# Kernel optimization log

Hardware: AMD Instinct MI355X
Metric: run time of the kernel (lower is better)

The kernel has to match this reference:

```python
import jax, jax.numpy as jnp
import numpy as np

EMBD_DIM = 1024
NUM_HEADS = 16
HEAD_DIM = EMBD_DIM // NUM_HEADS


def setup_inputs() -> dict:
    key = jax.random.key(0)
    ks = jax.random.split(key, 9)
    B, S, D = 2, 2048, EMBD_DIM
    scale = 1.0 / np.sqrt(D)
    return {
        "x": jax.random.normal(ks[0], (B, S, D), dtype=jnp.float32),
        "wq": jax.random.normal(ks[1], (D, D), dtype=jnp.float32) * scale,
        "bq": jnp.zeros((D,), dtype=jnp.float32),
        "wk": jax.random.normal(ks[2], (D, D), dtype=jnp.float32) * scale,
        "bk": jnp.zeros((D,), dtype=jnp.float32),
        "wv": jax.random.normal(ks[3], (D, D), dtype=jnp.float32) * scale,
        "bv": jnp.zeros((D,), dtype=jnp.float32),
        "wo": jax.random.normal(ks[4], (D, D), dtype=jnp.float32) * scale,
        "bo": jnp.zeros((D,), dtype=jnp.float32),
    }


def reference(x, wq, bq, wk, bk, wv, bv, wo, bo):
    B, S, D = x.shape
    H, hd = NUM_HEADS, HEAD_DIM
    # projections: weights stored as (in, out) so y = x @ w + b
    q = (x @ wq + bq).reshape(B, S, H, hd).transpose(0, 2, 1, 3)  # [B,H,S,hd]
    k = (x @ wk + bk).reshape(B, S, H, hd).transpose(0, 2, 1, 3)
    v = (x @ wv + bv).reshape(B, S, H, hd).transpose(0, 2, 1, 3)
    scores = jnp.einsum("bhqd,bhkd->bhqk", q, k) / jnp.sqrt(jnp.float32(hd))
    causal = jnp.tril(jnp.ones((S, S), dtype=bool))  # [S,S]
    neg = jnp.finfo(scores.dtype).min
    scores = jnp.where(causal[None, None, :, :], scores, neg)
    attn = jax.nn.softmax(scores, axis=-1)
    out = jnp.einsum("bhqk,bhkd->bhqd", attn, v)  # [B,H,S,hd]
    out = out.transpose(0, 2, 1, 3).reshape(B, S, D)
    return out @ wo + bo
```

## Files before the change

kernel.cpp:

```cpp
#include <hip/hip_runtime.h>
#include <math.h>

#define S_LEN 2048
#define BATCH 2
#define DMODEL 1024
#define NHEADS 16
#define MROWS 4096

typedef short bf8 __attribute__((ext_vector_type(8)));
typedef float f32x4 __attribute__((ext_vector_type(4)));
typedef unsigned short u16;

static __device__ inline u16 f2bf(float f) {
    union { float f; unsigned u; } v; v.f = f;
    unsigned r = v.u + 0x7fffu + ((v.u >> 16) & 1u);
    return (u16)(r >> 16);
}

static __device__ inline void load16(const void* g, void* l) {
    __builtin_amdgcn_global_load_lds(
        (const __attribute__((address_space(1))) unsigned int*)g,
        (__attribute__((address_space(3))) unsigned int*)l, 16, 0, 0);
}

__global__ __launch_bounds__(256) void prep_kernel(
    const float* __restrict__ x, u16* __restrict__ xb,
    const float* __restrict__ W0, const float* __restrict__ W1,
    const float* __restrict__ W2, const float* __restrict__ W3,
    u16* __restrict__ wT) {
    const int bx = blockIdx.x, t = threadIdx.x;
    if (bx < 2048) {
        int i = bx * 256 + t;
        const float4* p = (const float4*)x + (size_t)i * 2;
        float4 a = p[0], b = p[1];
        u16 tmp[8] = {f2bf(a.x), f2bf(a.y), f2bf(a.z), f2bf(a.w),
                      f2bf(b.x), f2bf(b.y), f2bf(b.z), f2bf(b.w)};
        ((uint4*)xb)[i] = *(uint4*)tmp;
        return;
    }
    __shared__ u16 Ls[64][65];
    const int id = bx - 2048;
    const int z = id >> 8, rem = id & 255;
    const int n0 = (rem & 15) * 64, k0 = (rem >> 4) * 64;
    const float* W = z == 0 ? W0 : z == 1 ? W1 : z == 2 ? W2 : W3;
    u16* Wt = wT + (size_t)z * 1024 * 1024;
    const int r = t >> 2, c4 = (t & 3) * 16;
    const float* p = W + (size_t)(k0 + r) * 1024 + n0 + c4;
#pragma unroll
    for (int i = 0; i < 16; i += 4) {
        float4 v = *(const float4*)(p + i);
        Ls[r][c4 + i + 0] = f2bf(v.x);
        Ls[r][c4 + i + 1] = f2bf(v.y);
        Ls[r][c4 + i + 2] = f2bf(v.z);
        Ls[r][c4 + i + 3] = f2bf(v.w);
    }
    __syncthreads();
    u16 tmp[16];
#pragma unroll
    for (int i = 0; i < 16; i++) tmp[i] = Ls[c4 + i][r];
    uint4* q = (uint4*)(Wt + (size_t)(n0 + r) * 1024 + k0 + c4);
    q[0] = *(uint4*)tmp;
    q[1] = *(uint4*)(tmp + 8);
}

template <int MODE>
__global__ __launch_bounds__(256) void gemm_mfma(
    const u16* __restrict__ A, const u16* __restrict__ Bt,
    const float* __restrict__ bqp, const float* __restrict__ bkp,
    const float* __restrict__ bvp,
    u16* __restrict__ qout, u16* __restrict__ kout, u16* __restrict__ vtout,
    float* __restrict__ fout, float qscale) {
    constexpr int TM = (MODE == 1) ? 64 : 128;
    constexpr int MI = (MODE == 1) ? 2 : 4;
    __shared__ __align__(16) u16 As[TM * 32];
    __shared__ __align__(16) u16 Bs[128 * 32];

    const int t = threadIdx.x, lane = t & 63, w = t >> 6;
    const int quad = lane >> 4, l16 = lane & 15;
    const int row0 = blockIdx.y * TM, col0 = blockIdx.x * 128;
    const int fq = (MODE == 1) ? w * 32 : (w & 1) * 64;
    const int xq = (MODE == 1) ? 0 : (w >> 1) * 64;
    const int K = DMODEL;

    const int koff = (((lane & 3) ^ ((lane >> 3) & 3))) * 8;
    const int srowA = (MODE == 1) ? (w * 16 + (lane >> 2)) : (w * 32 + (lane >> 2));
    const int srowB = w * 32 + (lane >> 2);
    const u16* ag = A + (size_t)(row0 + srowA) * K + koff;
    const u16* bg = Bt + (size_t)(col0 + srowB) * K + koff;
    u16* lA0 = As + ((MODE == 1) ? (w * 16) : (w * 32)) * 32;
    u16* lA1 = As + (w * 32 + 16) * 32;
    u16* lB0 = Bs + (w * 32) * 32;
    u16* lB1 = Bs + (w * 32 + 16) * 32;
    const size_t r16 = (size_t)16 * K;

    const int swz = (l16 >> 1) & 3;

    f32x4 acc[MI][4] = {};

    for (int k0 = 0; k0 < K; k0 += 32) {
        load16(ag + k0, lA0);
        if (MODE == 0) load16(ag + r16 + k0, lA1);
        load16(bg + k0, lB0);
        load16(bg + r16 + k0, lB1);
        __syncthreads();
        bf8 xf[4], wf[MI];
#pragma unroll
        for (int ni = 0; ni < 4; ni++)
            xf[ni] = *(const bf8*)&As[(xq + ni * 16 + l16) * 32 + (quad ^ swz) * 8];
#pragma unroll
        for (int mi = 0; mi < MI; mi++)
            wf[mi] = *(const bf8*)&Bs[(fq + mi * 16 + l16) * 32 + (quad ^ swz) * 8];
#pragma unroll
        for (int mi = 0; mi < MI; mi++)
#pragma unroll
            for (int ni = 0; ni < 4; ni++)
                acc[mi][ni] = __builtin_amdgcn_mfma_f32_16x16x32_bf16(
                    wf[mi], xf[ni], acc[mi][ni], 0, 0, 0);
        __syncthreads();
    }

    const int sect = (col0 + fq) >> 10;
#pragma unroll
    for (int mi = 0; mi < MI; mi++) {
        const int featb = col0 + fq + mi * 16 + quad * 4;
        float b4[4];
#pragma unroll
        for (int reg = 0; reg < 4; reg++)
            b4[reg] = (MODE == 1 ? bqp : (sect == 0 ? bqp : sect == 1 ? bkp : bvp))
                          [(featb + reg) & 1023];
#pragma unroll
        for (int ni = 0; ni < 4; ni++) {
            const int xrow = row0 + xq + ni * 16 + l16;
            if (MODE == 1) {
                float4 o;
                o.x = acc[mi][ni][0] + b4[0];
                o.y = acc[mi][ni][1] + b4[1];
                o.z = acc[mi][ni][2] + b4[2];
                o.w = acc[mi][ni][3] + b4[3];
                *(float4*)(fout + (size_t)xrow * 1024 + featb) = o;
            } else {
                const int cf = featb & 1023;
                if (sect == 0) {
                    u16 t4[4];
#pragma unroll
                    for (int reg = 0; reg < 4; reg++)
                        t4[reg] = f2bf((acc[mi][ni][reg] + b4[reg]) * qscale);
                    *(uint2*)(qout + (size_t)xrow * 1024 + cf) = *(uint2*)t4;
                } else if (sect == 1) {
                    u16 t4[4];
#pragma unroll
                    for (int reg = 0; reg < 4; reg++)
                        t4[reg] = f2bf(acc[mi][ni][reg] + b4[reg]);
                    *(uint2*)(kout + (size_t)xrow * 1024 + cf) = *(uint2*)t4;
                } else {
#pragma unroll
                    for (int reg = 0; reg < 4; reg++)
                        vtout[((size_t)(xrow >> 11) * 1024 + cf + reg) * S_LEN +
                              (xrow & 2047)] = f2bf(acc[mi][ni][reg] + b4[reg]);
                }
            }
        }
    }
}

__global__ __launch_bounds__(256) void attn_kernel(const u16* __restrict__ Qg,
                                                   const u16* __restrict__ Kg,
                                                   const u16* __restrict__ Vt,
                                                   u16* __restrict__ Og) {
    __shared__ __align__(16) u16 Ks[2][128][32];
    __shared__ __align__(16) u16 Vs[4][64][32];
    __shared__ __align__(16) u16 Ps[4][16][128];

    const int t = threadIdx.x, lane = t & 63, w = t >> 6;
    const int quad = lane >> 4, l16 = lane & 15;
    const int pi = blockIdx.x;
    const int bh = blockIdx.y, b = bh >> 4, h = bh & 15;
    const size_t base = (size_t)b * S_LEN * DMODEL + h * 64;
    const size_t vbase = ((size_t)b * 1024 + h * 64) * S_LEN;
    const int sr = t >> 2, sc = (t & 3) * 16;
    const int pl = sc >> 5;
    const int g0 = (sc >> 3) & 3;
    const int ss = (sr >> 1) & 3;
    const int swz = (l16 >> 1) & 3;

    const u16* kp = Kg + base + (size_t)sr * DMODEL + sc;
    const u16* vp = Vt + vbase + (size_t)sr * S_LEN + sc;
    const size_t kr64 = (size_t)64 * DMODEL;

    uint4 k0r = *(const uint4*)kp, k1r = *(const uint4*)(kp + 8);
    uint4 k2r = *(const uint4*)(kp + kr64), k3r = *(const uint4*)(kp + kr64 + 8);
    uint4 v0r = *(const uint4*)vp, v1r = *(const uint4*)(vp + 8);
    uint4 v2r = *(const uint4*)(vp + 64), v3r = *(const uint4*)(vp + 72);

#pragma unroll
    for (int seg = 0; seg < 2; seg++) {
        const int qt = seg == 0 ? pi : 31 - pi;
        const int niter = qt + 1;
        const int nd = (niter + 1) >> 1;
        const int q0 = qt * 64;

        bf8 aq[2];
#pragma unroll
        for (int c = 0; c < 2; c++)
            aq[c] = *(const bf8*)(Qg + base +
                (size_t)(q0 + w * 16 + l16) * DMODEL + c * 32 + quad * 8);

        float lsum[4] = {};
        f32x4 o_acc[4] = {};

        for (int j = 0; j < nd; j++) {
            __syncthreads();
            *(uint4*)&Ks[pl][sr][(g0 ^ ss) * 8] = k0r;
            *(uint4*)&Ks[pl][sr][((g0 + 1) ^ ss) * 8] = k1r;
            *(uint4*)&Ks[pl][sr + 64][(g0 ^ ss) * 8] = k2r;
            *(uint4*)&Ks[pl][sr + 64][((g0 + 1) ^ ss) * 8] = k3r;
            *(uint4*)&Vs[pl][sr][(g0 ^ ss) * 8] = v0r;
            *(uint4*)&Vs[pl][sr][((g0 + 1) ^ ss) * 8] = v1r;
            *(uint4*)&Vs[2 + pl][sr][(g0 ^ ss) * 8] = v2r;
            *(uint4*)&Vs[2 + pl][sr][((g0 + 1) ^ ss) * 8] = v3r;
            __syncthreads();

            if (j + 1 < nd || seg == 0) {
                size_t ok = (j + 1 < nd) ? (size_t)(j + 1) * 128 * DMODEL : 0;
                int ov = (j + 1 < nd) ? (j + 1) * 128 : 0;
                k0r = *(const uint4*)(kp + ok);
                k1r = *(const uint4*)(kp + ok + 8);
                k2r = *(const uint4*)(kp + ok + kr64);
                k3r = *(const uint4*)(kp + ok + kr64 + 8);
                v0r = *(const uint4*)(vp + ov);
                v1r = *(const uint4*)(vp + ov + 8);
                v2r = *(const uint4*)(vp + ov + 64);
                v3r = *(const uint4*)(vp + ov + 72);
            }

            f32x4 scv[8] = {};
#pragma unroll
            for (int c = 0; c < 2; c++)
#pragma unroll
                for (int ns = 0; ns < 8; ns++) {
                    bf8 bk = *(const bf8*)&Ks[c][ns * 16 + l16][(quad ^ swz) * 8];
                    scv[ns] = __builtin_amdgcn_mfma_f32_16x16x32_bf16(
                        aq[c], bk, scv[ns], 0, 0, 0);
                }

            const bool lastd = (j == nd - 1);
            const int qbase = q0 + w * 16 + quad * 4;
#pragma unroll
            for (int ns = 0; ns < 8; ns++) {
                const int key_g = j * 128 + ns * 16 + l16;
                const int g = ns * 2 + (l16 >> 3);
#pragma unroll
                for (int r = 0; r < 4; r++) {
                    float p = (lastd && key_g > qbase + r)
                                  ? 0.f
                                  : __builtin_amdgcn_exp2f(scv[ns][r]);
                    lsum[r] += p;
                    const int q = quad * 4 + r;
                    Ps[w][q][(g ^ (q & 7)) * 8 + (l16 & 7)] =
                        (u16)(__float_as_uint(p) >> 16);
                }
            }
            asm volatile("s_waitcnt lgkmcnt(0)" ::: "memory");

#pragma unroll
            for (int kk = 0; kk < 4; kk++) {
                bf8 apv = *(const bf8*)&Ps[w][l16][((kk * 4 + quad) ^ (l16 & 7)) * 8];
#pragma unroll
                for (int ds = 0; ds < 4; ds++) {
                    bf8 bvv = *(const bf8*)&Vs[kk][ds * 16 + l16][(quad ^ swz) * 8];
                    o_acc[ds] = __builtin_amdgcn_mfma_f32_16x16x32_bf16(
                        apv, bvv, o_acc[ds], 0, 0, 0);
                }
            }
        }

#pragma unroll
        for (int r = 0; r < 4; r++) {
            float l = lsum[r];
#pragma unroll
            for (int off = 8; off >= 1; off >>= 1) l += __shfl_xor(l, off, 64);
            float inv = 1.f / l;
            int qq = q0 + w * 16 + quad * 4 + r;
#pragma unroll
            for (int ds = 0; ds < 4; ds++)
                Og[base + (size_t)qq * DMODEL + ds * 16 + l16] =
                    f2bf(o_acc[ds][r] * inv);
        }
    }
}

extern "C" void kernel_launch(void* const* d_in, const int* in_sizes, int n_in,
                              void* d_out, int out_size, void* d_ws, size_t ws_size,
                              hipStream_t stream) {
    const float* x  = (const float*)d_in[0];
    const float* wq = (const float*)d_in[1];
    const float* bq = (const float*)d_in[2];
    const float* wk = (const float*)d_in[3];
    const float* bk = (const float*)d_in[4];
    const float* wv = (const float*)d_in[5];
    const float* bv = (const float*)d_in[6];
    const float* wo = (const float*)d_in[7];
    const float* bo = (const float*)d_in[8];
    float* out = (float*)d_out;

    const size_t E = (size_t)MROWS * DMODEL;
    u16* xb  = (u16*)d_out;
    u16* vt  = xb + E;
    u16* wT  = (u16*)d_ws;
    u16* woT = wT + 3145728;
    u16* qb  = wT + 4194304;
    u16* kb  = qb + E;
    u16* ob  = kb + E;

    dim3 blk(256);
    prep_kernel<<<3072, blk, 0, stream>>>(x, xb, wq, wk, wv, wo, wT);

    gemm_mfma<0><<<dim3(24, 32), blk, 0, stream>>>(
        xb, wT, bq, bk, bv, qb, kb, vt, nullptr, 0.18033688011112042f);

    dim3 agrid(16, BATCH * NHEADS);
    attn_kernel<<<agrid, blk, 0, stream>>>(qb, kb, vt, ob);

    gemm_mfma<1><<<dim3(8, 64), blk, 0, stream>>>(
        ob, woT, bo, nullptr, nullptr, nullptr, nullptr, nullptr, out, 1.0f);
}
```

Baseline: 207.0 us.

## Keep attention probabilities in registers via transposed MFMA and deepen GEMM K-tile

```diff
diff --git a/kernel.cpp b/kernel.cpp
--- a/kernel.cpp
+++ b/kernel.cpp
@@ -8,6 +8,7 @@
 #define MROWS 4096
 
 typedef short bf8 __attribute__((ext_vector_type(8)));
+typedef short bf4 __attribute__((ext_vector_type(4)));
 typedef float f32x4 __attribute__((ext_vector_type(4)));
 typedef unsigned short u16;
 
@@ -72,8 +73,9 @@
     float* __restrict__ fout, float qscale) {
     constexpr int TM = (MODE == 1) ? 64 : 128;
     constexpr int MI = (MODE == 1) ? 2 : 4;
-    __shared__ __align__(16) u16 As[TM * 32];
-    __shared__ __align__(16) u16 Bs[128 * 32];
+    constexpr int ADMA = (MODE == 1) ? 2 : 4;
+    __shared__ __align__(16) u16 As[TM * 64];
+    __shared__ __align__(16) u16 Bs[128 * 64];
 
     const int t = threadIdx.x, lane = t & 63, w = t >> 6;
     const int quad = lane >> 4, l16 = lane & 15;
@@ -82,40 +84,43 @@
     const int xq = (MODE == 1) ? 0 : (w >> 1) * 64;
     const int K = DMODEL;
 
-    const int koff = (((lane & 3) ^ ((lane >> 3) & 3))) * 8;
-    const int srowA = (MODE == 1) ? (w * 16 + (lane >> 2)) : (w * 32 + (lane >> 2));
-    const int srowB = w * 32 + (lane >> 2);
-    const u16* ag = A + (size_t)(row0 + srowA) * K + koff;
-    const u16* bg = Bt + (size_t)(col0 + srowB) * K + koff;
-    u16* lA0 = As + ((MODE == 1) ? (w * 16) : (w * 32)) * 32;
-    u16* lA1 = As + (w * 32 + 16) * 32;
-    u16* lB0 = Bs + (w * 32) * 32;
-    u16* lB1 = Bs + (w * 32 + 16) * 32;
-    const size_t r16 = (size_t)16 * K;
-
-    const int swz = (l16 >> 1) & 3;
+    const int lrow = lane >> 3;
+    const int koff = ((lane & 7) ^ lrow) * 8;
+    const int abase = (MODE == 1) ? w * 16 : w * 32;
+    const u16* ag = A + (size_t)(row0 + abase + lrow) * K + koff;
+    const u16* bg = Bt + (size_t)(col0 + w * 32 + lrow) * K + koff;
+    u16* lA = As + abase * 64;
+    u16* lB = Bs + (w * 32) * 64;
+    const int swz = l16 & 7;
 
     f32x4 acc[MI][4] = {};
 
-    for (int k0 = 0; k0 < K; k0 += 32) {
-        load16(ag + k0, lA0);
-        if (MODE == 0) load16(ag + r16 + k0, lA1);
-        load16(bg + k0, lB0);
-        load16(bg + r16 + k0, lB1);
+    for (int k0 = 0; k0 < K; k0 += 64) {
+#pragma unroll
+        for (int d = 0; d < ADMA; d++)
+            load16(ag + (size_t)d * 8 * K + k0, lA + d * 512);
+#pragma unroll
+        for (int d = 0; d < 4; d++)
+            load16(bg + (size_t)d * 8 * K + k0, lB + d * 512);
         __syncthreads();
-        bf8 xf[4], wf[MI];
-#pragma unroll
-        for (int ni = 0; ni < 4; ni++)
-            xf[ni] = *(const bf8*)&As[(xq + ni * 16 + l16) * 32 + (quad ^ swz) * 8];
-#pragma unroll
-        for (int mi = 0; mi < MI; mi++)
-            wf[mi] = *(const bf8*)&Bs[(fq + mi * 16 + l16) * 32 + (quad ^ swz) * 8];
-#pragma unroll
-        for (int mi = 0; mi < MI; mi++)
+#pragma unroll
+        for (int kc = 0; kc < 2; kc++) {
+            bf8 xf[4], wf[MI];
 #pragma unroll
             for (int ni = 0; ni < 4; ni++)
-                acc[mi][ni] = __builtin_amdgcn_mfma_f32_16x16x32_bf16(
-                    wf[mi], xf[ni], acc[mi][ni], 0, 0, 0);
+                xf[ni] = *(const bf8*)&As[(xq + ni * 16 + l16) * 64 +
+                                          ((kc * 4 + quad) ^ swz) * 8];
+#pragma unroll
+            for (int mi = 0; mi < MI; mi++)
+                wf[mi] = *(const bf8*)&Bs[(fq + mi * 16 + l16) * 64 +
+                                          ((kc * 4 + quad) ^ swz) * 8];
+#pragma unroll
+            for (int mi = 0; mi < MI; mi++)
+#pragma unroll
+                for (int ni = 0; ni < 4; ni++)
+                    acc[mi][ni] = __builtin_amdgcn_mfma_f32_16x16x32_bf16(
+                        wf[mi], xf[ni], acc[mi][ni], 0, 0, 0);
+        }
         __syncthreads();
     }
 
@@ -167,9 +172,8 @@
                                                    const u16* __restrict__ Kg,
                                                    const u16* __restrict__ Vt,
                                                    u16* __restrict__ Og) {
-    __shared__ __align__(16) u16 Ks[2][128][32];
-    __shared__ __align__(16) u16 Vs[4][64][32];
-    __shared__ __align__(16) u16 Ps[4][16][128];
+    __shared__ __align__(16) u16 Ks[2][64][32];
+    __shared__ __align__(16) u16 Vs[2][64][32];
 
     const int t = threadIdx.x, lane = t & 63, w = t >> 6;
     const int quad = lane >> 4, l16 = lane & 15;
@@ -185,18 +189,13 @@
 
     const u16* kp = Kg + base + (size_t)sr * DMODEL + sc;
     const u16* vp = Vt + vbase + (size_t)sr * S_LEN + sc;
-    const size_t kr64 = (size_t)64 * DMODEL;
-
     uint4 k0r = *(const uint4*)kp, k1r = *(const uint4*)(kp + 8);
-    uint4 k2r = *(const uint4*)(kp + kr64), k3r = *(const uint4*)(kp + kr64 + 8);
     uint4 v0r = *(const uint4*)vp, v1r = *(const uint4*)(vp + 8);
-    uint4 v2r = *(const uint4*)(vp + 64), v3r = *(const uint4*)(vp + 72);
 
 #pragma unroll
     for (int seg = 0; seg < 2; seg++) {
         const int qt = seg == 0 ? pi : 31 - pi;
         const int niter = qt + 1;
-        const int nd = (niter + 1) >> 1;
         const int q0 = qt * 64;
 
         bf8 aq[2];
@@ -205,86 +204,73 @@
             aq[c] = *(const bf8*)(Qg + base +
                 (size_t)(q0 + w * 16 + l16) * DMODEL + c * 32 + quad * 8);
 
-        float lsum[4] = {};
-        f32x4 o_acc[4] = {};
-
-        for (int j = 0; j < nd; j++) {
+        float lsum = 0.f;
+        f32x4 oT[4] = {};
+
+        for (int kt = 0; kt < niter; kt++) {
             __syncthreads();
             *(uint4*)&Ks[pl][sr][(g0 ^ ss) * 8] = k0r;
             *(uint4*)&Ks[pl][sr][((g0 + 1) ^ ss) * 8] = k1r;
-            *(uint4*)&Ks[pl][sr + 64][(g0 ^ ss) * 8] = k2r;
-            *(uint4*)&Ks[pl][sr + 64][((g0 + 1) ^ ss) * 8] = k3r;
             *(uint4*)&Vs[pl][sr][(g0 ^ ss) * 8] = v0r;
             *(uint4*)&Vs[pl][sr][((g0 + 1) ^ ss) * 8] = v1r;
-            *(uint4*)&Vs[2 + pl][sr][(g0 ^ ss) * 8] = v2r;
-            *(uint4*)&Vs[2 + pl][sr][((g0 + 1) ^ ss) * 8] = v3r;
             __syncthreads();
-
-            if (j + 1 < nd || seg == 0) {
-                size_t ok = (j + 1 < nd) ? (size_t)(j + 1) * 128 * DMODEL : 0;
-                int ov = (j + 1 < nd) ? (j + 1) * 128 : 0;
-                k0r = *(const uint4*)(kp + ok);
-                k1r = *(const uint4*)(kp + ok + 8);
-                k2r = *(const uint4*)(kp + ok + kr64);
-                k3r = *(const uint4*)(kp + ok + kr64 + 8);
-                v0r = *(const uint4*)(vp + ov);
-                v1r = *(const uint4*)(vp + ov + 8);
-                v2r = *(const uint4*)(vp + ov + 64);
-                v3r = *(const uint4*)(vp + ov + 72);
+            if (!(seg == 1 && kt + 1 == niter)) {
+                int nt = (kt + 1 < niter) ? kt + 1 : 0;
+                size_t ok = (size_t)nt * 64 * DMODEL;
+                int ov = nt * 64;
+                k0r = *(const uint4*)(kp + ok); k1r = *(const uint4*)(kp + ok + 8);
+                v0r = *(const uint4*)(vp + ov); v1r = *(const uint4*)(vp + ov + 8);
             }
 
-            f32x4 scv[8] = {};
+            f32x4 scv[4] = {};
 #pragma unroll
             for (int c = 0; c < 2; c++)
 #pragma unroll
-                for (int ns = 0; ns < 8; ns++) {
-                    bf8 bk = *(const bf8*)&Ks[c][ns * 16 + l16][(quad ^ swz) * 8];
+                for (int ns = 0; ns < 4; ns++) {
+                    bf8 ak = *(const bf8*)&Ks[c][ns * 16 + l16][(quad ^ swz) * 8];
                     scv[ns] = __builtin_amdgcn_mfma_f32_16x16x32_bf16(
-                        aq[c], bk, scv[ns], 0, 0, 0);
+                        ak, aq[c], scv[ns], 0, 0, 0);
                 }
 
-            const bool lastd = (j == nd - 1);
-            const int qbase = q0 + w * 16 + quad * 4;
-#pragma unroll
-            for (int ns = 0; ns < 8; ns++) {
-                const int key_g = j * 128 + ns * 16 + l16;
-                const int g = ns * 2 + (l16 >> 3);
+            const bool diag = (kt == qt);
+            const int ql = w * 16 + l16;
+#pragma unroll
+            for (int ns = 0; ns < 4; ns++) {
+                float p[4];
 #pragma unroll
                 for (int r = 0; r < 4; r++) {
-                    float p = (lastd && key_g > qbase + r)
-                                  ? 0.f
-                                  : __builtin_amdgcn_exp2f(scv[ns][r]);
-                    lsum[r] += p;
-                    const int q = quad * 4 + r;
-                    Ps[w][q][(g ^ (q & 7)) * 8 + (l16 & 7)] =
-                        (u16)(__float_as_uint(p) >> 16);
+                    int key = ns * 16 + quad * 4 + r;
+                    p[r] = (diag && key > ql) ? 0.f
+                                              : __builtin_amdgcn_exp2f(scv[ns][r]);
+                    lsum += p[r];
                 }
-            }
-            asm volatile("s_waitcnt lgkmcnt(0)" ::: "memory");
-
-#pragma unroll
-            for (int kk = 0; kk < 4; kk++) {
-                bf8 apv = *(const bf8*)&Ps[w][l16][((kk * 4 + quad) ^ (l16 & 7)) * 8];
+                union { unsigned u[2]; bf4 v; } pk;
+                pk.u[0] = (__float_as_uint(p[0]) >> 16) |
+                          (__float_as_uint(p[1]) & 0xffff0000u);
+                pk.u[1] = (__float_as_uint(p[2]) >> 16) |
+                          (__float_as_uint(p[3]) & 0xffff0000u);
 #pragma unroll
                 for (int ds = 0; ds < 4; ds++) {
-                    bf8 bvv = *(const bf8*)&Vs[kk][ds * 16 + l16][(quad ^ swz) * 8];
-                    o_acc[ds] = __builtin_amdgcn_mfma_f32_16x16x32_bf16(
-                        apv, bvv, o_acc[ds], 0, 0, 0);
+                    bf4 av = *(const bf4*)&Vs[ns >> 1][ds * 16 + l16]
+                        [((((ns & 1) * 2 + (quad >> 1)) ^ swz) * 8) + (quad & 1) * 4];
+                    oT[ds] = __builtin_amdgcn_mfma_f32_16x16x16bf16_1k(
+                        av, pk.v, oT[ds], 0, 0, 0);
                 }
             }
         }
 
-#pragma unroll
-        for (int r = 0; r < 4; r++) {
-            float l = lsum[r];
-#pragma unroll
-            for (int off = 8; off >= 1; off >>= 1) l += __shfl_xor(l, off, 64);
-            float inv = 1.f / l;
-            int qq = q0 + w * 16 + quad * 4 + r;
-#pragma unroll
-            for (int ds = 0; ds < 4; ds++)
-                Og[base + (size_t)qq * DMODEL + ds * 16 + l16] =
-                    f2bf(o_acc[ds][r] * inv);
+        float l = lsum;
+        l += __shfl_xor(l, 16, 64);
+        l += __shfl_xor(l, 32, 64);
+        const float inv = 1.f / l;
+        const int qq = q0 + w * 16 + l16;
+#pragma unroll
+        for (int ds = 0; ds < 4; ds++) {
+            u16 t4[4];
+#pragma unroll
+            for (int r = 0; r < 4; r++) t4[r] = f2bf(oT[ds][r] * inv);
+            *(uint2*)(Og + base + (size_t)qq * DMODEL + ds * 16 + quad * 4) =
+                *(uint2*)t4;
         }
     }
 }
```

New measurement: 197.4 us. -4.7%, faster.
